# Optimization experiments

Hardware: AMD Instinct MI355X
Metric: run time of the kernel (lower is better)

Reference implementation:

```python
import jax, jax.numpy as jnp
import numpy as np

B, N, D = 65536, 512, 512


def setup_inputs() -> dict:
    key = jax.random.key(0)
    k1, k2 = jax.random.split(key)
    # sample_orthonormal_vectors(n, d): QR of a (d, n) gaussian matrix, rows are codes
    rm = np.asarray(jax.random.normal(k1, (D, N), dtype=jnp.float32))
    Q, _ = np.linalg.qr(rm, mode='complete')  # Q: (d, d)
    codebook_vectors = jnp.asarray(Q.T[:, :N].T, dtype=jnp.float32)  # (n, d), w = 1.0
    batch_z = jax.random.normal(k2, (B, D), dtype=jnp.float32)
    return {"batch_z": batch_z, "codebook_vectors": codebook_vectors}


def reference(batch_z, codebook_vectors):
    """Faithful jax version of Codebook.closest_z.

    torch code materializes a (B, n, d) broadcast diff then norms over dim=2.
    Same math via the expanded squared-distance identity (no (B,n,d) tensor):
      ||z - c||^2 = ||z||^2 + ||c||^2 - 2 z.c
    """
    n, d = codebook_vectors.shape
    z = batch_z.reshape(-1, d)  # (B, d)
    z_sq = jnp.sum(z * z, axis=1, keepdims=True)                # (B, 1)
    c_sq = jnp.sum(codebook_vectors * codebook_vectors, axis=1)  # (n,)
    sq_dist = z_sq + c_sq[None, :] - 2.0 * (z @ codebook_vectors.T)  # (B, n)
    distances = jnp.sqrt(jnp.maximum(sq_dist, 0.0))
    indices = jnp.argmin(distances, axis=1)                      # (B,)
    one_hot = jax.nn.one_hot(indices, n, dtype=jnp.float32)      # eye(n)[indices]
    return one_hot, indices
```

## Files before the change

kernel.cpp:

```cpp
#include <hip/hip_runtime.h>
#include <math.h>

#define BQ 65536
#define NC 512
#define DD 512
#define BM 128
#define BN 256
#define BK 32
#define MARGIN 3e-3f
#define FINF 3.402823466e38f

typedef short bf16x8 __attribute__((ext_vector_type(8)));
typedef float f32x4 __attribute__((ext_vector_type(4)));

#define AHI 0
#define ALO 2560
#define STRIDE 20

__device__ __forceinline__ unsigned int cvt_pk_bf16(float a, float b) {
    unsigned int r;
    asm("v_cvt_pk_bf16_f32 %0, %1, %2" : "=v"(r) : "v"(a), "v"(b));
    return r;
}

__device__ __forceinline__ void split4(float4 v, uint2* hi, uint2* lo) {
    unsigned int h0 = cvt_pk_bf16(v.x, v.y);
    unsigned int h1 = cvt_pk_bf16(v.z, v.w);
    float hx = __uint_as_float(h0 << 16);
    float hy = __uint_as_float(h0 & 0xFFFF0000u);
    float hz = __uint_as_float(h1 << 16);
    float hw = __uint_as_float(h1 & 0xFFFF0000u);
    *hi = make_uint2(h0, h1);
    *lo = make_uint2(cvt_pk_bf16(v.x - hx, v.y - hy),
                     cvt_pk_bf16(v.z - hz, v.w - hw));
}

__device__ __forceinline__ void cvt8(float4 f0, float4 f1,
                                     bf16x8* hi, bf16x8* lo) {
    unsigned int h01 = cvt_pk_bf16(f0.x, f0.y);
    unsigned int h23 = cvt_pk_bf16(f0.z, f0.w);
    unsigned int h45 = cvt_pk_bf16(f1.x, f1.y);
    unsigned int h67 = cvt_pk_bf16(f1.z, f1.w);
    float a0 = __uint_as_float(h01 << 16), a1 = __uint_as_float(h01 & 0xFFFF0000u);
    float a2 = __uint_as_float(h23 << 16), a3 = __uint_as_float(h23 & 0xFFFF0000u);
    float a4 = __uint_as_float(h45 << 16), a5 = __uint_as_float(h45 & 0xFFFF0000u);
    float a6 = __uint_as_float(h67 << 16), a7 = __uint_as_float(h67 & 0xFFFF0000u);
    union { bf16x8 v; unsigned int u[4]; } H, L;
    H.u[0] = h01; H.u[1] = h23; H.u[2] = h45; H.u[3] = h67;
    L.u[0] = cvt_pk_bf16(f0.x - a0, f0.y - a1);
    L.u[1] = cvt_pk_bf16(f0.z - a2, f0.w - a3);
    L.u[2] = cvt_pk_bf16(f1.x - a4, f1.y - a5);
    L.u[3] = cvt_pk_bf16(f1.z - a6, f1.w - a7);
    *hi = H.v; *lo = L.v;
}

__device__ __forceinline__ float pw128_sq(const float* __restrict__ p) {
    float r[8];
    #pragma unroll
    for (int j = 0; j < 8; ++j) r[j] = 0.0f;
    #pragma unroll
    for (int q = 0; q < 32; ++q) {
        float4 v = *(const float4*)(p + q * 4);
        const int e = (q & 1) << 2;
        r[e + 0] = __fadd_rn(r[e + 0], __fmul_rn(v.x, v.x));
        r[e + 1] = __fadd_rn(r[e + 1], __fmul_rn(v.y, v.y));
        r[e + 2] = __fadd_rn(r[e + 2], __fmul_rn(v.z, v.z));
        r[e + 3] = __fadd_rn(r[e + 3], __fmul_rn(v.w, v.w));
    }
    return __fadd_rn(__fadd_rn(__fadd_rn(r[0], r[1]), __fadd_rn(r[2], r[3])),
                     __fadd_rn(__fadd_rn(r[4], r[5]), __fadd_rn(r[6], r[7])));
}

__global__ __launch_bounds__(256, 2) void codebook_kernel(
    const float* __restrict__ Z, const float* __restrict__ Cb,
    float* __restrict__ out, int* __restrict__ wslist, int cap) {

    __shared__ __align__(16) unsigned int stage[5120];
    __shared__ float csq[NC];
    __shared__ float red_b1[2][BM];
    __shared__ float red_b2[2][BM];
    __shared__ int   red_i1[2][BM];
    __shared__ int   bif[BM];

    const int tid = threadIdx.x;
    const int m0 = blockIdx.x * BM;
    const int l = tid & 63, wid = tid >> 6;
    const int wr0 = (wid >> 1) * 64;
    const int wc0 = (wid & 1) * 128;
    const int g = l >> 4, c = l & 15;

    #pragma unroll
    for (int cc = 0; cc < 2; ++cc) {
        const int code = tid + cc * 256;
        const float* p = Cb + (size_t)code * DD;
        float b0 = pw128_sq(p), b1 = pw128_sq(p + 128);
        float b2 = pw128_sq(p + 256), b3 = pw128_sq(p + 384);
        csq[code] = __fadd_rn(__fadd_rn(b0, b1), __fadd_rn(b2, b3));
    }

    float rb1 = FINF, rb2 = FINF; int ri1 = 0;

    float4 va[4];
    #pragma unroll
    for (int p = 0; p < 4; ++p) {
        int q = tid + p * 256;
        va[p] = *(const float4*)(Z + (size_t)(m0 + (q >> 3)) * DD + (q & 7) * 4);
    }
    float4 ring[8];
    #pragma unroll
    for (int j = 0; j < 4; ++j) {
        int C = wc0 + j * 16 + c;
        ring[2 * j]     = *(const float4*)(Cb + (size_t)C * DD + g * 8);
        ring[2 * j + 1] = *(const float4*)(Cb + (size_t)C * DD + g * 8 + 4);
    }

    f32x4 acc[4][8];

    for (int step = 0; step < 32; ++step) {
        const int n0 = (step >> 4) * BN;
        const int kt = (step & 15) * BK;
        const int nstep = (step < 31) ? step + 1 : 31;
        const int ktn = (nstep & 15) * BK;
        const int n0n = (nstep >> 4) * BN;

        if ((step & 15) == 0) {
            #pragma unroll
            for (int i = 0; i < 4; ++i)
                #pragma unroll
                for (int j = 0; j < 8; ++j) acc[i][j] = (f32x4)0.0f;
        }
        __syncthreads();
        #pragma unroll
        for (int p = 0; p < 4; ++p) {
            int q = tid + p * 256;
            int r = q >> 3, k2 = (q & 7) * 2;
            uint2 h, lo;
            split4(va[p], &h, &lo);
            *(uint2*)&stage[AHI + r * STRIDE + k2] = h;
            *(uint2*)&stage[ALO + r * STRIDE + k2] = lo;
        }
        __syncthreads();
        if (step < 31) {
            #pragma unroll
            for (int p = 0; p < 4; ++p) {
                int q = tid + p * 256;
                va[p] = *(const float4*)(Z + (size_t)(m0 + (q >> 3)) * DD + ktn + (q & 7) * 4);
            }
        }
        bf16x8 ah[4], al[4];
        #pragma unroll
        for (int i = 0; i < 4; ++i) {
            int R = wr0 + i * 16 + c;
            ah[i] = *(bf16x8*)&stage[AHI + R * STRIDE + g * 4];
            al[i] = *(bf16x8*)&stage[ALO + R * STRIDE + g * 4];
        }
        #pragma unroll
        for (int j = 0; j < 8; ++j) {
            bf16x8 bh, bl;
            cvt8(ring[2 * (j & 3)], ring[2 * (j & 3) + 1], &bh, &bl);
            {
                const int jj = (j < 4) ? (j + 4) : (j - 4);
                const int kk = (j < 4) ? kt : ktn;
                const int nn = (j < 4) ? n0 : n0n;
                const int C = nn + wc0 + jj * 16 + c;
                ring[2 * (j & 3)]     = *(const float4*)(Cb + (size_t)C * DD + kk + g * 8);
                ring[2 * (j & 3) + 1] = *(const float4*)(Cb + (size_t)C * DD + kk + g * 8 + 4);
            }
            #pragma unroll
            for (int i = 0; i < 4; ++i) {
                acc[i][j] = __builtin_amdgcn_mfma_f32_16x16x32_bf16(ah[i], bh, acc[i][j], 0, 0, 0);
                acc[i][j] = __builtin_amdgcn_mfma_f32_16x16x32_bf16(ah[i], bl, acc[i][j], 0, 0, 0);
                acc[i][j] = __builtin_amdgcn_mfma_f32_16x16x32_bf16(al[i], bh, acc[i][j], 0, 0, 0);
            }
        }

        if ((step & 15) == 15) {
            #pragma unroll
            for (int i = 0; i < 4; ++i) {
                #pragma unroll
                for (int r = 0; r < 4; ++r) {
                    float b1 = FINF, b2 = FINF; int i1 = 0;
                    #pragma unroll
                    for (int j = 0; j < 8; ++j) {
                        int code = n0 + wc0 + j * 16 + c;
                        float m = fmaf(-2.0f, acc[i][j][r], csq[code]);
                        if (m < b1) { b2 = b1; b1 = m; i1 = code; }
                        else b2 = fminf(b2, m);
                    }
                    #pragma unroll
                    for (int s = 1; s < 16; s <<= 1) {
                        float ob1 = __shfl_xor(b1, s);
                        float ob2 = __shfl_xor(b2, s);
                        int oi1 = __shfl_xor(i1, s);
                        if (ob1 < b1 || (ob1 == b1 && oi1 < i1)) {
                            b2 = fminf(b1, ob2); b1 = ob1; i1 = oi1;
                        } else {
                            b2 = fminf(b2, ob1);
                        }
                    }
                    if (c == 0) {
                        int row = wr0 + i * 16 + g * 4 + r;
                        red_b1[wid & 1][row] = b1;
                        red_b2[wid & 1][row] = b2;
                        red_i1[wid & 1][row] = i1;
                    }
                }
            }
            __syncthreads();
            if (tid < BM) {
                #pragma unroll
                for (int h = 0; h < 2; ++h) {
                    float nb1 = red_b1[h][tid], nb2 = red_b2[h][tid];
                    int ni = red_i1[h][tid];
                    if (nb1 < rb1) { rb2 = fminf(rb1, nb2); rb1 = nb1; ri1 = ni; }
                    else rb2 = fminf(rb2, nb1);
                }
            }
        }
    }

    if (tid < BM) {
        bif[tid] = ri1;
        out[(size_t)BQ * NC + m0 + tid] = (float)ri1;
        if (rb2 - rb1 < MARGIN) {
            int slot = atomicAdd(wslist, 1);
            if (slot < cap) wslist[1 + slot] = m0 + tid;
        }
    }
    __syncthreads();

    #pragma unroll 4
    for (int t = 0; t < 64; ++t) {
        int f4i = tid + t * 256;
        int r = f4i >> 7, c4 = f4i & 127;
        int tgt = bif[r];
        int base = c4 * 4;
        float4 v;
        v.x = (tgt == base + 0) ? 1.0f : 0.0f;
        v.y = (tgt == base + 1) ? 1.0f : 0.0f;
        v.z = (tgt == base + 2) ? 1.0f : 0.0f;
        v.w = (tgt == base + 3) ? 1.0f : 0.0f;
        *(float4*)(out + (size_t)(m0 + r) * NC + (size_t)base) = v;
    }
}

__global__ __launch_bounds__(256) void fixup_kernel(
    const float* __restrict__ Z, const float* __restrict__ Cb,
    float* __restrict__ out, const int* __restrict__ wslist, int cap) {

    __shared__ float zrow[DD];
    __shared__ double md[256];
    __shared__ int mi[256];
    const int tid = threadIdx.x;
    int count = wslist[0];
    if (count > cap) count = cap;

    for (int e = blockIdx.x; e < count; e += gridDim.x) {
        const int row = wslist[1 + e];
        zrow[tid] = Z[(size_t)row * DD + tid];
        zrow[tid + 256] = Z[(size_t)row * DD + 256 + tid];
        __syncthreads();

        double bb = 1e300; int bidx = 0;
        #pragma unroll
        for (int cc = 0; cc < 2; ++cc) {
            const int code = tid * 2 + cc;
            const float* cp = Cb + (size_t)code * DD;
            double dot = 0.0, cs = 0.0;
            for (int k = 0; k < DD; k += 4) {
                float4 c4 = *(const float4*)(cp + k);
                double a0 = (double)zrow[k + 0], c0 = (double)c4.x;
                double a1 = (double)zrow[k + 1], c1 = (double)c4.y;
                double a2 = (double)zrow[k + 2], c2 = (double)c4.z;
                double a3 = (double)zrow[k + 3], c3 = (double)c4.w;
                dot = fma(a0, c0, dot); cs = fma(c0, c0, cs);
                dot = fma(a1, c1, dot); cs = fma(c1, c1, cs);
                dot = fma(a2, c2, dot); cs = fma(c2, c2, cs);
                dot = fma(a3, c3, dot); cs = fma(c3, c3, cs);
            }
            double m = cs - 2.0 * dot;
            if (m < bb || (m == bb && code < bidx)) { bb = m; bidx = code; }
        }
        md[tid] = bb; mi[tid] = bidx;
        __syncthreads();
        for (int s = 128; s > 0; s >>= 1) {
            if (tid < s) {
                if (md[tid + s] < md[tid] ||
                    (md[tid + s] == md[tid] && mi[tid + s] < mi[tid])) {
                    md[tid] = md[tid + s]; mi[tid] = mi[tid + s];
                }
            }
            __syncthreads();
        }
        const int imin = mi[0];
        out[(size_t)row * NC + tid] = (tid == imin) ? 1.0f : 0.0f;
        out[(size_t)row * NC + 256 + tid] = (tid + 256 == imin) ? 1.0f : 0.0f;
        if (tid == 0) out[(size_t)BQ * NC + row] = (float)imin;
        __syncthreads();
    }
}

extern "C" void kernel_launch(void* const* d_in, const int* in_sizes, int n_in,
                              void* d_out, int out_size, void* d_ws, size_t ws_size,
                              hipStream_t stream) {
    const float* Z = (const float*)d_in[0];
    const float* Cb = (const float*)d_in[1];
    float* out = (float*)d_out;
    int* wslist = (int*)d_ws;
    int cap = (int)(ws_size / 4) - 1;
    if (cap > BQ) cap = BQ;
    hipMemsetAsync(d_ws, 0, 4, stream);
    codebook_kernel<<<dim3(BQ / BM), dim3(256), 0, stream>>>(Z, Cb, out, wslist, cap);
    fixup_kernel<<<dim3(512), dim3(256), 0, stream>>>(Z, Cb, out, wslist, cap);
}
```

Baseline: 319.6 us.

## Halve row tile, double-buffer A in LDS, raise occupancy to 4 blocks

Shrinks the row tile from 128 to 64 so each of the four waves covers all 64 rows and a 64-code slice, which halves the per-wave accumulator count. A double-buffered bf16 hi/lo staging area in shared memory lets the next K-slice be split and written while the current one is consumed, cutting one of the two barriers per step. Launch bounds move to 4 blocks per CU to hide latency, at the cost of codebook fragments being reloaded by twice as many blocks and a four-way cross-wave reduction.

```diff
diff --git a/kernel.cpp b/kernel.cpp
--- a/kernel.cpp
+++ b/kernel.cpp
@@ -4,18 +4,16 @@
 #define BQ 65536
 #define NC 512
 #define DD 512
-#define BM 128
+#define BM 64
 #define BN 256
 #define BK 32
 #define MARGIN 3e-3f
 #define FINF 3.402823466e38f
 
+#define ASTR 40
+
 typedef short bf16x8 __attribute__((ext_vector_type(8)));
 typedef float f32x4 __attribute__((ext_vector_type(4)));
-
-#define AHI 0
-#define ALO 2560
-#define STRIDE 20
 
 __device__ __forceinline__ unsigned int cvt_pk_bf16(float a, float b) {
     unsigned int r;
@@ -71,23 +69,24 @@
                      __fadd_rn(__fadd_rn(r[4], r[5]), __fadd_rn(r[6], r[7])));
 }
 
-__global__ __launch_bounds__(256, 2) void codebook_kernel(
+__global__ __launch_bounds__(256, 4) void codebook_kernel(
     const float* __restrict__ Z, const float* __restrict__ Cb,
     float* __restrict__ out, int* __restrict__ wslist, int cap) {
 
-    __shared__ __align__(16) unsigned int stage[5120];
+    __shared__ __align__(16) unsigned short Ahi[2][BM * ASTR];
+    __shared__ __align__(16) unsigned short Alo[2][BM * ASTR];
     __shared__ float csq[NC];
-    __shared__ float red_b1[2][BM];
-    __shared__ float red_b2[2][BM];
-    __shared__ int   red_i1[2][BM];
+    __shared__ float red_b1[4][BM];
+    __shared__ float red_b2[4][BM];
+    __shared__ int   red_i1[4][BM];
     __shared__ int   bif[BM];
 
     const int tid = threadIdx.x;
     const int m0 = blockIdx.x * BM;
     const int l = tid & 63, wid = tid >> 6;
-    const int wr0 = (wid >> 1) * 64;
-    const int wc0 = (wid & 1) * 128;
+    const int wc0 = wid * 64;
     const int g = l >> 4, c = l & 15;
+    const int ar = tid >> 2, akq = tid & 3;
 
     #pragma unroll
     for (int cc = 0; cc < 2; ++cc) {
@@ -100,71 +99,77 @@
 
     float rb1 = FINF, rb2 = FINF; int ri1 = 0;
 
-    float4 va[4];
+    float4 va0, va1;
+    {
+        const float* zp = Z + (size_t)(m0 + ar) * DD + akq * 8;
+        va0 = *(const float4*)zp;
+        va1 = *(const float4*)(zp + 4);
+        uint2 h0, l0, h1, l1;
+        split4(va0, &h0, &l0);
+        split4(va1, &h1, &l1);
+        *(uint4*)&Ahi[0][ar * ASTR + akq * 8] = make_uint4(h0.x, h0.y, h1.x, h1.y);
+        *(uint4*)&Alo[0][ar * ASTR + akq * 8] = make_uint4(l0.x, l0.y, l1.x, l1.y);
+        zp = Z + (size_t)(m0 + ar) * DD + BK + akq * 8;
+        va0 = *(const float4*)zp;
+        va1 = *(const float4*)(zp + 4);
+    }
+    float4 ring[4];
     #pragma unroll
-    for (int p = 0; p < 4; ++p) {
-        int q = tid + p * 256;
-        va[p] = *(const float4*)(Z + (size_t)(m0 + (q >> 3)) * DD + (q & 7) * 4);
-    }
-    float4 ring[8];
-    #pragma unroll
-    for (int j = 0; j < 4; ++j) {
+    for (int j = 0; j < 2; ++j) {
         int C = wc0 + j * 16 + c;
         ring[2 * j]     = *(const float4*)(Cb + (size_t)C * DD + g * 8);
         ring[2 * j + 1] = *(const float4*)(Cb + (size_t)C * DD + g * 8 + 4);
     }
-
-    f32x4 acc[4][8];
+    __syncthreads();
+
+    f32x4 acc[4][4];
+    int cur = 0;
 
     for (int step = 0; step < 32; ++step) {
         const int n0 = (step >> 4) * BN;
-        const int kt = (step & 15) * BK;
-        const int nstep = (step < 31) ? step + 1 : 31;
-        const int ktn = (nstep & 15) * BK;
-        const int n0n = (nstep >> 4) * BN;
+        const int t1 = (step < 31) ? step + 1 : 31;
+        const int ktn = (t1 & 15) * BK, n0n = (t1 >> 4) * BN;
+        const int t2 = (step < 30) ? step + 2 : 31;
+        const int kt2 = (t2 & 15) * BK;
+        const int nxt = cur ^ 1;
 
         if ((step & 15) == 0) {
             #pragma unroll
             for (int i = 0; i < 4; ++i)
                 #pragma unroll
-                for (int j = 0; j < 8; ++j) acc[i][j] = (f32x4)0.0f;
-        }
-        __syncthreads();
-        #pragma unroll
-        for (int p = 0; p < 4; ++p) {
-            int q = tid + p * 256;
-            int r = q >> 3, k2 = (q & 7) * 2;
-            uint2 h, lo;
-            split4(va[p], &h, &lo);
-            *(uint2*)&stage[AHI + r * STRIDE + k2] = h;
-            *(uint2*)&stage[ALO + r * STRIDE + k2] = lo;
-        }
-        __syncthreads();
-        if (step < 31) {
-            #pragma unroll
-            for (int p = 0; p < 4; ++p) {
-                int q = tid + p * 256;
-                va[p] = *(const float4*)(Z + (size_t)(m0 + (q >> 3)) * DD + ktn + (q & 7) * 4);
-            }
-        }
+                for (int j = 0; j < 4; ++j) acc[i][j] = (f32x4)0.0f;
+        }
+
         bf16x8 ah[4], al[4];
         #pragma unroll
         for (int i = 0; i < 4; ++i) {
-            int R = wr0 + i * 16 + c;
-            ah[i] = *(bf16x8*)&stage[AHI + R * STRIDE + g * 4];
-            al[i] = *(bf16x8*)&stage[ALO + R * STRIDE + g * 4];
-        }
+            int R = i * 16 + c;
+            ah[i] = *(bf16x8*)&Ahi[cur][R * ASTR + g * 8];
+            al[i] = *(bf16x8*)&Alo[cur][R * ASTR + g * 8];
+        }
+
+        {
+            uint2 h0, l0, h1, l1;
+            split4(va0, &h0, &l0);
+            split4(va1, &h1, &l1);
+            *(uint4*)&Ahi[nxt][ar * ASTR + akq * 8] = make_uint4(h0.x, h0.y, h1.x, h1.y);
+            *(uint4*)&Alo[nxt][ar * ASTR + akq * 8] = make_uint4(l0.x, l0.y, l1.x, l1.y);
+            const float* zp = Z + (size_t)(m0 + ar) * DD + kt2 + akq * 8;
+            va0 = *(const float4*)zp;
+            va1 = *(const float4*)(zp + 4);
+        }
+
         #pragma unroll
-        for (int j = 0; j < 8; ++j) {
+        for (int j = 0; j < 4; ++j) {
             bf16x8 bh, bl;
-            cvt8(ring[2 * (j & 3)], ring[2 * (j & 3) + 1], &bh, &bl);
+            cvt8(ring[2 * (j & 1)], ring[2 * (j & 1) + 1], &bh, &bl);
             {
-                const int jj = (j < 4) ? (j + 4) : (j - 4);
-                const int kk = (j < 4) ? kt : ktn;
-                const int nn = (j < 4) ? n0 : n0n;
+                const int jj = (j < 2) ? (j + 2) : (j - 2);
+                const int kk = (j < 2) ? ((step & 15) * BK) : ktn;
+                const int nn = (j < 2) ? n0 : n0n;
                 const int C = nn + wc0 + jj * 16 + c;
-                ring[2 * (j & 3)]     = *(const float4*)(Cb + (size_t)C * DD + kk + g * 8);
-                ring[2 * (j & 3) + 1] = *(const float4*)(Cb + (size_t)C * DD + kk + g * 8 + 4);
+                ring[2 * (j & 1)]     = *(const float4*)(Cb + (size_t)C * DD + kk + g * 8);
+                ring[2 * (j & 1) + 1] = *(const float4*)(Cb + (size_t)C * DD + kk + g * 8 + 4);
             }
             #pragma unroll
             for (int i = 0; i < 4; ++i) {
@@ -181,7 +186,7 @@
                 for (int r = 0; r < 4; ++r) {
                     float b1 = FINF, b2 = FINF; int i1 = 0;
                     #pragma unroll
-                    for (int j = 0; j < 8; ++j) {
+                    for (int j = 0; j < 4; ++j) {
                         int code = n0 + wc0 + j * 16 + c;
                         float m = fmaf(-2.0f, acc[i][j][r], csq[code]);
                         if (m < b1) { b2 = b1; b1 = m; i1 = code; }
@@ -199,17 +204,17 @@
                         }
                     }
                     if (c == 0) {
-                        int row = wr0 + i * 16 + g * 4 + r;
-                        red_b1[wid & 1][row] = b1;
-                        red_b2[wid & 1][row] = b2;
-                        red_i1[wid & 1][row] = i1;
+                        int row = i * 16 + g * 4 + r;
+                        red_b1[wid][row] = b1;
+                        red_b2[wid][row] = b2;
+                        red_i1[wid][row] = i1;
                     }
                 }
             }
             __syncthreads();
             if (tid < BM) {
                 #pragma unroll
-                for (int h = 0; h < 2; ++h) {
+                for (int h = 0; h < 4; ++h) {
                     float nb1 = red_b1[h][tid], nb2 = red_b2[h][tid];
                     int ni = red_i1[h][tid];
                     if (nb1 < rb1) { rb2 = fminf(rb1, nb2); rb1 = nb1; ri1 = ni; }
@@ -217,6 +222,9 @@
                 }
             }
         }
+
+        __syncthreads();
+        cur = nxt;
     }
 
     if (tid < BM) {
@@ -230,7 +238,7 @@
     __syncthreads();
 
     #pragma unroll 4
-    for (int t = 0; t < 64; ++t) {
+    for (int t = 0; t < 32; ++t) {
         int f4i = tid + t * 256;
         int r = f4i >> 7, c4 = f4i & 127;
         int tgt = bif[r];
```

After: 435.1 us. 1.36x slower.
